# Kernel optimization log

Hardware: AMD Instinct MI355X
Metric: run time of the kernel (lower is better)

Reference implementation:

```python
import jax, jax.numpy as jnp
import numpy as np

NOISE_STD = 0.1
TOP_K = 2

def setup_inputs() -> dict:
    key = jax.random.key(0)
    k1, k2, k3, k4 = jax.random.split(key, 4)
    B, S, H = 4, 4096, 2048
    E, SE, NS = 64, 64, 10
    x = jax.random.normal(k1, (B, S, H), dtype=jnp.float32)
    scale_embeddings = jax.random.normal(k2, (NS, SE), dtype=jnp.float32)
    # nn.Linear(H+SE, E, bias=False) weight: [E, H+SE]
    router_w = jax.random.normal(k3, (E, H + SE), dtype=jnp.float32) / np.sqrt(H + SE).astype(np.float32)
    # pre-sampled standard-normal noise (training path), scaled by NOISE_STD inside reference
    noise = jax.random.normal(k4, (B, S, E), dtype=jnp.float32)
    return {"x": x, "scale_embeddings": scale_embeddings, "router_w": router_w,
            "noise": noise, "scale_idx": 3}

def reference(x, scale_embeddings, router_w, noise, scale_idx):
    B, S, _ = x.shape
    # scale_idx is not None branch: lookup one scale embedding, broadcast over tokens
    emb = scale_embeddings[scale_idx]                      # [SE]
    emb = jnp.broadcast_to(emb, (B, S, emb.shape[-1]))     # [B,S,SE]
    x_with_scale = jnp.concatenate([x, emb], axis=-1)      # [B,S,H+SE]
    # router: bias-free linear projection to expert logits
    router_logits = jnp.einsum('bsd,ed->bse', x_with_scale, router_w)
    router_logits = router_logits + noise * NOISE_STD      # training noise injection
    routing_probs = jax.nn.softmax(router_logits, axis=-1)  # [B,S,E]
    routing_weights, selected_experts = jax.lax.top_k(routing_probs, TOP_K)
    routing_weights = routing_weights / routing_weights.sum(axis=-1, keepdims=True)
    # scatter normalized weights into dense dispatch tensor [B,S,E]
    dispatch = (jax.nn.one_hot(selected_experts, routing_probs.shape[-1],
                               dtype=routing_probs.dtype)
                * routing_weights[..., None]).sum(axis=-2)
    return dispatch
```

## Files before the change

### kernel.cpp

```cpp
#include <hip/hip_runtime.h>
#include <hip/hip_bf16.h>
#include <math.h>
#include <stdint.h>


#define H_DIM 2048
#define K_TOTAL 2112
#define E_DIM 64
#define SE_DIM 64
#define NSTEP 64
#define NKR 8
#define KR_LEN 256
#define KS_PER_KR 8
#define TG_TOK 512
#define STEP_BYTES (12 * 1024)
#define WP_TOTAL (NSTEP * STEP_BYTES)
#define BSLICE_BYTES (KS_PER_KR * STEP_BYTES)
#define LOGITS_OFF (WP_TOTAL + 256)
#define LOGITS_BYTES (16384 * E_DIM * 4)

typedef float  f32x4 __attribute__((ext_vector_type(4)));
typedef short  s16x8 __attribute__((ext_vector_type(8)));
typedef unsigned int u32x4 __attribute__((ext_vector_type(4)));

typedef uint32_t __attribute__((address_space(1))) gu32_t;
typedef uint32_t __attribute__((address_space(3))) lu32_t;
__device__ __forceinline__ void gload_lds16(const void* g, void* l) {
    __builtin_amdgcn_global_load_lds((const gu32_t*)g, (lu32_t*)l, 16, 0, 0);
}

__device__ __forceinline__ unsigned short bf16_rne(float f) {
    uint32_t u = __float_as_uint(f);
    return (unsigned short)((u + 0x7FFFu + ((u >> 16) & 1u)) >> 16);
}
__device__ __forceinline__ float bf16_f32(unsigned short h) {
    return __uint_as_float(((uint32_t)h) << 16);
}
__device__ __forceinline__ uint32_t bits_of_bf2(__hip_bfloat162 h) {
    uint32_t u; __builtin_memcpy(&u, &h, 4); return u;
}

__global__ void prep_kernel(const float* __restrict__ W,
                            const float* __restrict__ se,
                            const int* __restrict__ sidx,
                            unsigned short* __restrict__ Wp,
                            float* __restrict__ tail) {
    if (blockIdx.x == 64) {
        int e = threadIdx.x;
        if (e < 64) {
            const float* emb = se + (*sidx) * SE_DIM;
            float t = 0.f;
            for (int j = 0; j < SE_DIM; ++j)
                t = fmaf(emb[j], W[(size_t)e * K_TOTAL + H_DIM + j], t);
            tail[e] = t;
        }
        return;
    }
    int item = blockIdx.x * 256 + threadIdx.x;
    int lane = item & 63;
    int nt   = (item >> 6) & 3;
    int s    = item >> 8;
    int e     = nt * 16 + (lane & 15);
    int kbase = s * 32 + (lane >> 4) * 8;
    const float* wr = W + (size_t)e * K_TOTAL + kbase;
    unsigned short p0[8], p1[8], p2[8];
    #pragma unroll
    for (int j = 0; j < 8; ++j) {
        float v = wr[j];
        unsigned short a0 = bf16_rne(v);
        float r1 = v - bf16_f32(a0);
        unsigned short a1 = bf16_rne(r1);
        float r2 = r1 - bf16_f32(a1);
        p0[j] = a0; p1[j] = a1; p2[j] = bf16_rne(r2);
    }
    size_t rec = (size_t)s * 12 + nt * 3;
    unsigned short* d0 = Wp + (rec + 0) * 512 + lane * 8;
    unsigned short* d1 = Wp + (rec + 1) * 512 + lane * 8;
    unsigned short* d2 = Wp + (rec + 2) * 512 + lane * 8;
    #pragma unroll
    for (int j = 0; j < 8; ++j) { d0[j] = p0[j]; d1[j] = p1[j]; d2[j] = p2[j]; }
}

__device__ __forceinline__ void split3(const float4 fa, const float4 fb,
                                       s16x8& P0, s16x8& P1, s16x8& P2) {
    float f[8] = {fa.x, fa.y, fa.z, fa.w, fb.x, fb.y, fb.z, fb.w};
    uint32_t d0[4], d1[4], d2[4];
    #pragma unroll
    for (int p = 0; p < 4; ++p) {
        float v0 = f[2 * p], v1 = f[2 * p + 1];
        uint32_t u0 = bits_of_bf2(__float22bfloat162_rn(make_float2(v0, v1)));
        float r0 = v0 - __uint_as_float(u0 << 16);
        float r1 = v1 - __uint_as_float(u0 & 0xffff0000u);
        uint32_t u1 = bits_of_bf2(__float22bfloat162_rn(make_float2(r0, r1)));
        float s0 = r0 - __uint_as_float(u1 << 16);
        float s1 = r1 - __uint_as_float(u1 & 0xffff0000u);
        uint32_t u2 = bits_of_bf2(__float22bfloat162_rn(make_float2(s0, s1)));
        d0[p] = u0; d1[p] = u1; d2[p] = u2;
    }
    u32x4 q0 = {d0[0], d0[1], d0[2], d0[3]};
    u32x4 q1 = {d1[0], d1[1], d1[2], d1[3]};
    u32x4 q2 = {d2[0], d2[1], d2[2], d2[3]};
    __builtin_memcpy(&P0, &q0, 16);
    __builtin_memcpy(&P1, &q1, 16);
    __builtin_memcpy(&P2, &q2, 16);
}

__launch_bounds__(512, 2)
__global__ void gemm_kernel(const float* __restrict__ x,
                            const unsigned char* __restrict__ Wp,
                            float* __restrict__ logits) {
    __shared__ __align__(16) unsigned char Bs[BSLICE_BYTES];

    const int tid  = threadIdx.x;
    const int lane = tid & 63;
    const int wave = __builtin_amdgcn_readfirstlane(tid >> 6);
    const int kr   = blockIdx.x >> 5;
    const int tg   = blockIdx.x & 31;
    const int row  = lane & 15;
    const int quad = lane >> 4;
    const int c    = row;

    {
        const unsigned char* bsrc = Wp + (size_t)kr * BSLICE_BYTES + tid * 16;
        #pragma unroll
        for (int i = 0; i < 12; ++i)
            gload_lds16(bsrc + i * 8192, &Bs[tid * 16 + i * 8192]);
        asm volatile("s_waitcnt vmcnt(0)" ::: "memory");
        __syncthreads();
    }

    const float* ap = x + (size_t)(tg * TG_TOK + wave * 64 + row) * H_DIM
                        + kr * KR_LEN + quad * 8;
    f32x4 acc0 = {0.f, 0.f, 0.f, 0.f}, acc1 = acc0, acc2 = acc0, acc3 = acc0;

    #define A_ADDR(J) (ap + (size_t)((J) >> 3) * (16 * H_DIM) + ((J) & 7) * 32)
    #define ISSUE(J, VA, VB) do {                                  \
        const float* _p = A_ADDR(J);                               \
        VA = *(const float4*)_p;                                   \
        VB = *(const float4*)(_p + 4);                             \
    } while (0)

    #define FLUSH(MT) do {                                                  \
        int tokb = tg * TG_TOK + wave * 64 + (MT) * 16 + quad * 4;          \
        float* lg = logits + (size_t)tokb * E_DIM + c;                      \
        _Pragma("unroll")                                                   \
        for (int r = 0; r < 4; ++r) {                                       \
            atomicAdd(lg + r * E_DIM +  0, acc0[r]);                        \
            atomicAdd(lg + r * E_DIM + 16, acc1[r]);                        \
            atomicAdd(lg + r * E_DIM + 32, acc2[r]);                        \
            atomicAdd(lg + r * E_DIM + 48, acc3[r]);                        \
        }                                                                   \
        f32x4 _z = {0.f, 0.f, 0.f, 0.f};                                    \
        acc0 = _z; acc1 = _z; acc2 = _z; acc3 = _z;                         \
    } while (0)

    #define COMPUTE(J, VA, VB) do {                                         \
        s16x8 A0, A1, A2;                                                   \
        split3(VA, VB, A0, A1, A2);                                         \
        const unsigned char* _bb = &Bs[((J) & 7) * STEP_BYTES + lane * 16]; \
        {                                                                   \
            s16x8 B0 = *(const s16x8*)(_bb);                                \
            s16x8 B1 = *(const s16x8*)(_bb + 1024);                         \
            s16x8 B2 = *(const s16x8*)(_bb + 2048);                         \
            acc0 = __builtin_amdgcn_mfma_f32_16x16x32_bf16(A0, B0, acc0, 0, 0, 0); \
            acc0 = __builtin_amdgcn_mfma_f32_16x16x32_bf16(A0, B1, acc0, 0, 0, 0); \
            acc0 = __builtin_amdgcn_mfma_f32_16x16x32_bf16(A1, B0, acc0, 0, 0, 0); \
            acc0 = __builtin_amdgcn_mfma_f32_16x16x32_bf16(A0, B2, acc0, 0, 0, 0); \
            acc0 = __builtin_amdgcn_mfma_f32_16x16x32_bf16(A1, B1, acc0, 0, 0, 0); \
            acc0 = __builtin_amdgcn_mfma_f32_16x16x32_bf16(A2, B0, acc0, 0, 0, 0); \
        }                                                                   \
        {                                                                   \
            s16x8 B0 = *(const s16x8*)(_bb + 3072);                         \
            s16x8 B1 = *(const s16x8*)(_bb + 4096);                         \
            s16x8 B2 = *(const s16x8*)(_bb + 5120);                         \
            acc1 = __builtin_amdgcn_mfma_f32_16x16x32_bf16(A0, B0, acc1, 0, 0, 0); \
            acc1 = __builtin_amdgcn_mfma_f32_16x16x32_bf16(A0, B1, acc1, 0, 0, 0); \
            acc1 = __builtin_amdgcn_mfma_f32_16x16x32_bf16(A1, B0, acc1, 0, 0, 0); \
            acc1 = __builtin_amdgcn_mfma_f32_16x16x32_bf16(A0, B2, acc1, 0, 0, 0); \
            acc1 = __builtin_amdgcn_mfma_f32_16x16x32_bf16(A1, B1, acc1, 0, 0, 0); \
            acc1 = __builtin_amdgcn_mfma_f32_16x16x32_bf16(A2, B0, acc1, 0, 0, 0); \
        }                                                                   \
        {                                                                   \
            s16x8 B0 = *(const s16x8*)(_bb + 6144);                         \
            s16x8 B1 = *(const s16x8*)(_bb + 7168);                         \
            s16x8 B2 = *(const s16x8*)(_bb + 8192);                         \
            acc2 = __builtin_amdgcn_mfma_f32_16x16x32_bf16(A0, B0, acc2, 0, 0, 0); \
            acc2 = __builtin_amdgcn_mfma_f32_16x16x32_bf16(A0, B1, acc2, 0, 0, 0); \
            acc2 = __builtin_amdgcn_mfma_f32_16x16x32_bf16(A1, B0, acc2, 0, 0, 0); \
            acc2 = __builtin_amdgcn_mfma_f32_16x16x32_bf16(A0, B2, acc2, 0, 0, 0); \
            acc2 = __builtin_amdgcn_mfma_f32_16x16x32_bf16(A1, B1, acc2, 0, 0, 0); \
            acc2 = __builtin_amdgcn_mfma_f32_16x16x32_bf16(A2, B0, acc2, 0, 0, 0); \
        }                                                                   \
        {                                                                   \
            s16x8 B0 = *(const s16x8*)(_bb + 9216);                         \
            s16x8 B1 = *(const s16x8*)(_bb + 10240);                        \
            s16x8 B2 = *(const s16x8*)(_bb + 11264);                        \
            acc3 = __builtin_amdgcn_mfma_f32_16x16x32_bf16(A0, B0, acc3, 0, 0, 0); \
            acc3 = __builtin_amdgcn_mfma_f32_16x16x32_bf16(A0, B1, acc3, 0, 0, 0); \
            acc3 = __builtin_amdgcn_mfma_f32_16x16x32_bf16(A1, B0, acc3, 0, 0, 0); \
            acc3 = __builtin_amdgcn_mfma_f32_16x16x32_bf16(A0, B2, acc3, 0, 0, 0); \
            acc3 = __builtin_amdgcn_mfma_f32_16x16x32_bf16(A1, B1, acc3, 0, 0, 0); \
            acc3 = __builtin_amdgcn_mfma_f32_16x16x32_bf16(A2, B0, acc3, 0, 0, 0); \
        }                                                                   \
        if (((J) & 7) == 7) FLUSH((J) >> 3);                                \
    } while (0)

    float4 a0_, b0_, a1_, b1_, a2_, b2_;
    ISSUE(0, a0_, b0_);
    ISSUE(1, a1_, b1_);
    #pragma unroll 1
    for (int it = 0; it < 10; ++it) {
        const int j = it * 3;
        ISSUE(j + 2, a2_, b2_);
        __builtin_amdgcn_sched_barrier(0);
        COMPUTE(j, a0_, b0_);
        ISSUE(j + 3, a0_, b0_);
        __builtin_amdgcn_sched_barrier(0);
        COMPUTE(j + 1, a1_, b1_);
        ISSUE(j + 4, a1_, b1_);
        __builtin_amdgcn_sched_barrier(0);
        COMPUTE(j + 2, a2_, b2_);
    }
    COMPUTE(30, a0_, b0_);
    COMPUTE(31, a1_, b1_);

    #undef COMPUTE
    #undef FLUSH
    #undef ISSUE
    #undef A_ADDR
}

__launch_bounds__(256, 4)
__global__ void finish_kernel(const float* __restrict__ logits,
                              const float* __restrict__ tail,
                              const float* __restrict__ noise,
                              float* __restrict__ out) {
    const int t = blockIdx.x * 256 + threadIdx.x;
    const float4* L4 = (const float4*)(logits + (size_t)t * E_DIM);
    const float4* N4 = (const float4*)(noise  + (size_t)t * E_DIM);
    const float4* T4 = (const float4*)tail;

    float V1 = -3.4e38f, V2 = -3.4e38f;
    int   I1 = 0x7fffffff, I2 = 0x7fffffff;
    #define UPD(V, E) do {                                          \
        float _v = (V); int _e = (E);                               \
        if (_v > V1)      { V2 = V1; I2 = I1; V1 = _v; I1 = _e; }   \
        else if (_v > V2) { V2 = _v; I2 = _e; }                     \
    } while (0)
    #pragma unroll
    for (int i = 0; i < 16; ++i) {
        float4 l = L4[i], n = N4[i], tl = T4[i];
        UPD(l.x + tl.x + 0.1f * n.x, i * 4 + 0);
        UPD(l.y + tl.y + 0.1f * n.y, i * 4 + 1);
        UPD(l.z + tl.z + 0.1f * n.z, i * 4 + 2);
        UPD(l.w + tl.w + 0.1f * n.w, i * 4 + 3);
    }
    #undef UPD
    float d   = expf(V2 - V1);
    float inv = 1.0f / (1.0f + d);
    float w1 = inv, w2 = d * inv;

    float4* O4 = (float4*)(out + (size_t)t * E_DIM);
    #pragma unroll
    for (int i = 0; i < 16; ++i) {
        int e = i * 4;
        float4 o;
        o.x = (e + 0 == I1) ? w1 : (e + 0 == I2) ? w2 : 0.0f;
        o.y = (e + 1 == I1) ? w1 : (e + 1 == I2) ? w2 : 0.0f;
        o.z = (e + 2 == I1) ? w1 : (e + 2 == I2) ? w2 : 0.0f;
        o.w = (e + 3 == I1) ? w1 : (e + 3 == I2) ? w2 : 0.0f;
        O4[i] = o;
    }
}

extern "C" void kernel_launch(void* const* d_in, const int* in_sizes, int n_in,
                              void* d_out, int out_size, void* d_ws, size_t ws_size,
                              hipStream_t stream) {
    const float* x     = (const float*)d_in[0];
    const float* se    = (const float*)d_in[1];
    const float* W     = (const float*)d_in[2];
    const float* noise = (const float*)d_in[3];
    const int*   sidx  = (const int*)d_in[4];
    float* out = (float*)d_out;

    unsigned short* Wp     = (unsigned short*)d_ws;
    float*          tail   = (float*)((char*)d_ws + WP_TOTAL);
    float*          logits = (float*)((char*)d_ws + LOGITS_OFF);

    hipMemsetAsync(logits, 0, LOGITS_BYTES, stream);
    hipLaunchKernelGGL(prep_kernel, dim3(65), dim3(256), 0, stream,
                       W, se, sidx, Wp, tail);
    hipLaunchKernelGGL(gemm_kernel, dim3(NKR * 32), dim3(512), 0, stream,
                       x, (const unsigned char*)Wp, logits);
    hipLaunchKernelGGL(finish_kernel, dim3(64), dim3(256), 0, stream,
                       logits, tail, noise, out);
}
```

Before: 220.6 us.

## Split K finer across more blocks and simplify GEMM loop; smaller finish blocks

The GEMM now splits K into 16 ranges of 128 instead of 8 of 256, giving 512 blocks of 256 threads, each holding half the LDS B slice. The software-pipelined A loads across steps are replaced by a simple loop that loads four k-steps of A at once and flushes accumulators with atomics after each 64-token tile. The finish kernel now uses 256 blocks of 64 threads to spread the tail work over more CUs. The goal is more parallelism and occupancy across CUs, at the cost of twice as many atomic adds into the logits and the loss of explicit cross-iteration load prefetching.

```diff
diff --git a/kernel.cpp b/kernel.cpp
--- a/kernel.cpp
+++ b/kernel.cpp
@@ -9,10 +9,9 @@
 #define E_DIM 64
 #define SE_DIM 64
 #define NSTEP 64
-#define NKR 8
-#define KR_LEN 256
-#define KS_PER_KR 8
-#define TG_TOK 512
+#define NKR 16
+#define KR_LEN 128
+#define KS_PER_KR 4
 #define STEP_BYTES (12 * 1024)
 #define WP_TOTAL (NSTEP * STEP_BYTES)
 #define BSLICE_BYTES (KS_PER_KR * STEP_BYTES)
@@ -105,7 +104,7 @@
     __builtin_memcpy(&P2, &q2, 16);
 }
 
-__launch_bounds__(512, 2)
+__launch_bounds__(256, 2)
 __global__ void gemm_kernel(const float* __restrict__ x,
                             const unsigned char* __restrict__ Wp,
                             float* __restrict__ logits) {
@@ -115,7 +114,7 @@
     const int lane = tid & 63;
     const int wave = __builtin_amdgcn_readfirstlane(tid >> 6);
     const int kr   = blockIdx.x >> 5;
-    const int tg   = blockIdx.x & 31;
+    const int tgs  = blockIdx.x & 31;
     const int row  = lane & 15;
     const int quad = lane >> 4;
     const int c    = row;
@@ -124,40 +123,18 @@
         const unsigned char* bsrc = Wp + (size_t)kr * BSLICE_BYTES + tid * 16;
         #pragma unroll
         for (int i = 0; i < 12; ++i)
-            gload_lds16(bsrc + i * 8192, &Bs[tid * 16 + i * 8192]);
+            gload_lds16(bsrc + i * 4096, &Bs[tid * 16 + i * 4096]);
         asm volatile("s_waitcnt vmcnt(0)" ::: "memory");
         __syncthreads();
     }
 
-    const float* ap = x + (size_t)(tg * TG_TOK + wave * 64 + row) * H_DIM
+    const float* ap = x + (size_t)(tgs * 512 + wave * 16 + row) * H_DIM
                         + kr * KR_LEN + quad * 8;
-    f32x4 acc0 = {0.f, 0.f, 0.f, 0.f}, acc1 = acc0, acc2 = acc0, acc3 = acc0;
-
-    #define A_ADDR(J) (ap + (size_t)((J) >> 3) * (16 * H_DIM) + ((J) & 7) * 32)
-    #define ISSUE(J, VA, VB) do {                                  \
-        const float* _p = A_ADDR(J);                               \
-        VA = *(const float4*)_p;                                   \
-        VB = *(const float4*)(_p + 4);                             \
-    } while (0)
-
-    #define FLUSH(MT) do {                                                  \
-        int tokb = tg * TG_TOK + wave * 64 + (MT) * 16 + quad * 4;          \
-        float* lg = logits + (size_t)tokb * E_DIM + c;                      \
-        _Pragma("unroll")                                                   \
-        for (int r = 0; r < 4; ++r) {                                       \
-            atomicAdd(lg + r * E_DIM +  0, acc0[r]);                        \
-            atomicAdd(lg + r * E_DIM + 16, acc1[r]);                        \
-            atomicAdd(lg + r * E_DIM + 32, acc2[r]);                        \
-            atomicAdd(lg + r * E_DIM + 48, acc3[r]);                        \
-        }                                                                   \
-        f32x4 _z = {0.f, 0.f, 0.f, 0.f};                                    \
-        acc0 = _z; acc1 = _z; acc2 = _z; acc3 = _z;                         \
-    } while (0)
-
-    #define COMPUTE(J, VA, VB) do {                                         \
+
+    #define COMPUTE(KS, VA, VB) do {                                        \
         s16x8 A0, A1, A2;                                                   \
         split3(VA, VB, A0, A1, A2);                                         \
-        const unsigned char* _bb = &Bs[((J) & 7) * STEP_BYTES + lane * 16]; \
+        const unsigned char* _bb = &Bs[(KS) * STEP_BYTES + lane * 16];      \
         {                                                                   \
             s16x8 B0 = *(const s16x8*)(_bb);                                \
             s16x8 B1 = *(const s16x8*)(_bb + 1024);                         \
@@ -202,40 +179,46 @@
             acc3 = __builtin_amdgcn_mfma_f32_16x16x32_bf16(A1, B1, acc3, 0, 0, 0); \
             acc3 = __builtin_amdgcn_mfma_f32_16x16x32_bf16(A2, B0, acc3, 0, 0, 0); \
         }                                                                   \
-        if (((J) & 7) == 7) FLUSH((J) >> 3);                                \
     } while (0)
 
-    float4 a0_, b0_, a1_, b1_, a2_, b2_;
-    ISSUE(0, a0_, b0_);
-    ISSUE(1, a1_, b1_);
     #pragma unroll 1
-    for (int it = 0; it < 10; ++it) {
-        const int j = it * 3;
-        ISSUE(j + 2, a2_, b2_);
+    for (int it = 0; it < 8; ++it) {
+        const float* a = ap + (size_t)it * (64 * H_DIM);
+        float4 A00 = *(const float4*)(a);
+        float4 A01 = *(const float4*)(a + 4);
+        float4 A10 = *(const float4*)(a + 32);
+        float4 A11 = *(const float4*)(a + 36);
+        float4 A20 = *(const float4*)(a + 64);
+        float4 A21 = *(const float4*)(a + 68);
+        float4 A30 = *(const float4*)(a + 96);
+        float4 A31 = *(const float4*)(a + 100);
         __builtin_amdgcn_sched_barrier(0);
-        COMPUTE(j, a0_, b0_);
-        ISSUE(j + 3, a0_, b0_);
-        __builtin_amdgcn_sched_barrier(0);
-        COMPUTE(j + 1, a1_, b1_);
-        ISSUE(j + 4, a1_, b1_);
-        __builtin_amdgcn_sched_barrier(0);
-        COMPUTE(j + 2, a2_, b2_);
-    }
-    COMPUTE(30, a0_, b0_);
-    COMPUTE(31, a1_, b1_);
-
+
+        f32x4 acc0 = {0.f, 0.f, 0.f, 0.f}, acc1 = acc0, acc2 = acc0, acc3 = acc0;
+        COMPUTE(0, A00, A01);
+        COMPUTE(1, A10, A11);
+        COMPUTE(2, A20, A21);
+        COMPUTE(3, A30, A31);
+
+        const int tokb = tgs * 512 + it * 64 + wave * 16 + quad * 4;
+        float* lg = logits + (size_t)tokb * E_DIM + c;
+        #pragma unroll
+        for (int r = 0; r < 4; ++r) {
+            atomicAdd(lg + r * E_DIM +  0, acc0[r]);
+            atomicAdd(lg + r * E_DIM + 16, acc1[r]);
+            atomicAdd(lg + r * E_DIM + 32, acc2[r]);
+            atomicAdd(lg + r * E_DIM + 48, acc3[r]);
+        }
+    }
     #undef COMPUTE
-    #undef FLUSH
-    #undef ISSUE
-    #undef A_ADDR
-}
-
-__launch_bounds__(256, 4)
+}
+
+__launch_bounds__(64, 4)
 __global__ void finish_kernel(const float* __restrict__ logits,
                               const float* __restrict__ tail,
                               const float* __restrict__ noise,
                               float* __restrict__ out) {
-    const int t = blockIdx.x * 256 + threadIdx.x;
+    const int t = blockIdx.x * 64 + threadIdx.x;
     const float4* L4 = (const float4*)(logits + (size_t)t * E_DIM);
     const float4* N4 = (const float4*)(noise  + (size_t)t * E_DIM);
     const float4* T4 = (const float4*)tail;
@@ -290,8 +273,8 @@
     hipMemsetAsync(logits, 0, LOGITS_BYTES, stream);
     hipLaunchKernelGGL(prep_kernel, dim3(65), dim3(256), 0, stream,
                        W, se, sidx, Wp, tail);
-    hipLaunchKernelGGL(gemm_kernel, dim3(NKR * 32), dim3(512), 0, stream,
+    hipLaunchKernelGGL(gemm_kernel, dim3(NKR * 32), dim3(256), 0, stream,
                        x, (const unsigned char*)Wp, logits);
-    hipLaunchKernelGGL(finish_kernel, dim3(64), dim3(256), 0, stream,
+    hipLaunchKernelGGL(finish_kernel, dim3(256), dim3(64), 0, stream,
                        logits, tail, noise, out);
 }
```

Result: slower. 232.7 us (+5.5%).
